# Performance work log

Measured on AMD Instinct MI355X. Metric: run time of the kernel, lower is better.

Reference implementation:

```python
import jax, jax.numpy as jnp
import numpy as np

DIM = 1024
NUM_HEADS = 16
HEAD_DIM = DIM // NUM_HEADS


def setup_inputs() -> dict:
    key = jax.random.key(0)
    k1, k2, k3, k4 = jax.random.split(key, 4)
    x = jax.random.normal(k1, (2, 2048, DIM), dtype=jnp.float32)
    # nn.Linear(dim, 3*dim, bias=False): weight [3*dim, dim], y = x @ W.T
    w_qkv = jax.random.normal(k2, (3 * DIM, DIM), dtype=jnp.float32) * (1.0 / np.sqrt(DIM))
    w_proj = jax.random.normal(k3, (DIM, DIM), dtype=jnp.float32) * (1.0 / np.sqrt(DIM))
    b_proj = jax.random.normal(k4, (DIM,), dtype=jnp.float32) * 0.02
    return {"x": x, "w_qkv": w_qkv, "w_proj": w_proj, "b_proj": b_proj}


def reference(x, w_qkv, w_proj, b_proj):
    B, N, C = x.shape
    H, D = NUM_HEADS, HEAD_DIM
    qkv = jnp.einsum('bnc,oc->bno', x, w_qkv)            # [B,N,3C]
    qkv = qkv.reshape(B, N, 3, H, D)
    q = jnp.transpose(qkv[:, :, 0], (0, 2, 1, 3))        # [B,H,N,D]
    k = jnp.transpose(qkv[:, :, 1], (0, 2, 1, 3))
    v = jnp.transpose(qkv[:, :, 2], (0, 2, 1, 3))
    scale = 1.0 / jnp.sqrt(jnp.asarray(D, dtype=x.dtype))
    scores = jnp.einsum('bhnd,bhmd->bhnm', q, k) * scale  # [B,H,N,N]
    attn = jax.nn.softmax(scores, axis=-1)
    o = jnp.einsum('bhnm,bhmd->bhnd', attn, v)            # [B,H,N,D]
    o = jnp.transpose(o, (0, 2, 1, 3)).reshape(B, N, C)
    return jnp.einsum('bnc,oc->bno', o, w_proj) + b_proj
```

## Files before the change

kernel.cpp:

```cpp
#include <hip/hip_runtime.h>
#include <cmath>

#define DIM 1024
#define NHEADS 16
#define HDIM 64
#define NB 2
#define SEQ 2048

typedef __bf16 bf16x8 __attribute__((ext_vector_type(8)));
typedef __bf16 bf16x4 __attribute__((ext_vector_type(4)));
typedef float f32x4 __attribute__((ext_vector_type(4)));

union Bf8 { bf16x8 v; __bf16 e[8]; unsigned short us[8]; };
union Bf4 { bf16x4 v; __bf16 e[4]; };

__device__ __forceinline__ void split_bf(float f, __bf16 &h, __bf16 &l) {
    h = (__bf16)f;
    l = (__bf16)(f - (float)h);
}
__device__ __forceinline__ unsigned int pack_bf(float f) {
    __bf16 h, l;
    split_bf(f, h, l);
    union { __bf16 b; unsigned short u; } ch, cl;
    ch.b = h; cl.b = l;
    return (unsigned int)ch.u | ((unsigned int)cl.u << 16);
}

__global__ __launch_bounds__(256) void split_f32(const float* __restrict__ in,
                                                 __bf16* __restrict__ hi,
                                                 __bf16* __restrict__ lo, int n4) {
    for (int i = blockIdx.x * blockDim.x + threadIdx.x; i < n4;
         i += gridDim.x * blockDim.x) {
        const float4 v = reinterpret_cast<const float4*>(in)[i];
        const float f[4] = {v.x, v.y, v.z, v.w};
        Bf4 h, l;
#pragma unroll
        for (int e = 0; e < 4; ++e) split_bf(f[e], h.e[e], l.e[e]);
        reinterpret_cast<bf16x4*>(hi)[i] = h.v;
        reinterpret_cast<bf16x4*>(lo)[i] = l.v;
    }
}

template <bool SA, bool SB, bool SOUT, bool QSCALE, bool HAS_BIAS>
__global__ __launch_bounds__(256) void gemm_nt_mfma(
    const float* __restrict__ Af, const __bf16* __restrict__ Agh, const __bf16* __restrict__ Agl,
    const float* __restrict__ Bf, const __bf16* __restrict__ Bgh, const __bf16* __restrict__ Bgl,
    const float* __restrict__ bias,
    float* __restrict__ Cf, __bf16* __restrict__ Cgh, __bf16* __restrict__ Cgl,
    int M, int Nc, int K) {
    __shared__ __align__(16) __bf16 Ah[128][40];
    __shared__ __align__(16) __bf16 Al[128][40];
    __shared__ __align__(16) __bf16 Bh[128][40];
    __shared__ __align__(16) __bf16 Bl[128][40];

    const int nwg  = gridDim.x;
    const int orig = blockIdx.x;
    const int tile = (orig & 7) * (nwg >> 3) + (orig >> 3);
    const int gx   = Nc >> 7;
    const int m0   = (tile / gx) * 128;
    const int n0   = (tile % gx) * 128;

    const int t  = threadIdx.x;
    const int w  = t >> 6;
    const int l  = t & 63;
    const int wr = (w >> 1) * 64;
    const int wc = (w & 1) * 64;
    const int lr = l & 15;
    const int kg = l >> 4;

    const int srow = t >> 1;
    const int skh  = (t & 1) * 16;
    const size_t arow = (size_t)(m0 + srow) * K + skh;
    const size_t brow = (size_t)(n0 + srow) * K + skh;

    f32x4 acc[4][4] = {};

    for (int k0 = 0; k0 < K; k0 += 32) {
        float4 av[4], bv[4];
        bf16x8 sah[2], sal[2], sbh[2], sbl[2];
        if constexpr (SA) {
            sah[0] = *reinterpret_cast<const bf16x8*>(Agh + arow + k0);
            sah[1] = *reinterpret_cast<const bf16x8*>(Agh + arow + k0 + 8);
            sal[0] = *reinterpret_cast<const bf16x8*>(Agl + arow + k0);
            sal[1] = *reinterpret_cast<const bf16x8*>(Agl + arow + k0 + 8);
        } else {
#pragma unroll
            for (int i = 0; i < 4; ++i)
                av[i] = *reinterpret_cast<const float4*>(Af + arow + k0 + i * 4);
        }
        if constexpr (SB) {
            sbh[0] = *reinterpret_cast<const bf16x8*>(Bgh + brow + k0);
            sbh[1] = *reinterpret_cast<const bf16x8*>(Bgh + brow + k0 + 8);
            sbl[0] = *reinterpret_cast<const bf16x8*>(Bgl + brow + k0);
            sbl[1] = *reinterpret_cast<const bf16x8*>(Bgl + brow + k0 + 8);
        } else {
#pragma unroll
            for (int i = 0; i < 4; ++i)
                bv[i] = *reinterpret_cast<const float4*>(Bf + brow + k0 + i * 4);
        }
        __syncthreads();

        if constexpr (SA) {
            *reinterpret_cast<bf16x8*>(&Ah[srow][skh])     = sah[0];
            *reinterpret_cast<bf16x8*>(&Ah[srow][skh + 8]) = sah[1];
            *reinterpret_cast<bf16x8*>(&Al[srow][skh])     = sal[0];
            *reinterpret_cast<bf16x8*>(&Al[srow][skh + 8]) = sal[1];
        } else {
#pragma unroll
            for (int half = 0; half < 2; ++half) {
                Bf8 hh, ll;
#pragma unroll
                for (int q = 0; q < 2; ++q) {
                    const float4 va = av[half * 2 + q];
                    const float fa[4] = {va.x, va.y, va.z, va.w};
#pragma unroll
                    for (int e = 0; e < 4; ++e)
                        split_bf(fa[e], hh.e[q * 4 + e], ll.e[q * 4 + e]);
                }
                *reinterpret_cast<bf16x8*>(&Ah[srow][skh + half * 8]) = hh.v;
                *reinterpret_cast<bf16x8*>(&Al[srow][skh + half * 8]) = ll.v;
            }
        }
        if constexpr (SB) {
            *reinterpret_cast<bf16x8*>(&Bh[srow][skh])     = sbh[0];
            *reinterpret_cast<bf16x8*>(&Bh[srow][skh + 8]) = sbh[1];
            *reinterpret_cast<bf16x8*>(&Bl[srow][skh])     = sbl[0];
            *reinterpret_cast<bf16x8*>(&Bl[srow][skh + 8]) = sbl[1];
        } else {
#pragma unroll
            for (int half = 0; half < 2; ++half) {
                Bf8 hh, ll;
#pragma unroll
                for (int q = 0; q < 2; ++q) {
                    const float4 vb = bv[half * 2 + q];
                    const float fb[4] = {vb.x, vb.y, vb.z, vb.w};
#pragma unroll
                    for (int e = 0; e < 4; ++e)
                        split_bf(fb[e], hh.e[q * 4 + e], ll.e[q * 4 + e]);
                }
                *reinterpret_cast<bf16x8*>(&Bh[srow][skh + half * 8]) = hh.v;
                *reinterpret_cast<bf16x8*>(&Bl[srow][skh + half * 8]) = ll.v;
            }
        }
        __syncthreads();

        bf16x8 fah[4], fal[4], fbh[4], fbl[4];
#pragma unroll
        for (int mi = 0; mi < 4; ++mi) {
            fah[mi] = *reinterpret_cast<const bf16x8*>(&Ah[wr + mi * 16 + lr][kg * 8]);
            fal[mi] = *reinterpret_cast<const bf16x8*>(&Al[wr + mi * 16 + lr][kg * 8]);
        }
#pragma unroll
        for (int nj = 0; nj < 4; ++nj) {
            fbh[nj] = *reinterpret_cast<const bf16x8*>(&Bh[wc + nj * 16 + lr][kg * 8]);
            fbl[nj] = *reinterpret_cast<const bf16x8*>(&Bl[wc + nj * 16 + lr][kg * 8]);
        }
#pragma unroll
        for (int mi = 0; mi < 4; ++mi)
#pragma unroll
            for (int nj = 0; nj < 4; ++nj) {
                acc[mi][nj] = __builtin_amdgcn_mfma_f32_16x16x32_bf16(
                    fah[mi], fbh[nj], acc[mi][nj], 0, 0, 0);
                acc[mi][nj] = __builtin_amdgcn_mfma_f32_16x16x32_bf16(
                    fal[mi], fbh[nj], acc[mi][nj], 0, 0, 0);
                acc[mi][nj] = __builtin_amdgcn_mfma_f32_16x16x32_bf16(
                    fah[mi], fbl[nj], acc[mi][nj], 0, 0, 0);
            }
    }

    const int orw = kg * 4;
#pragma unroll
    for (int mi = 0; mi < 4; ++mi) {
#pragma unroll
        for (int r = 0; r < 4; ++r) {
            const int row = m0 + wr + mi * 16 + orw + r;
#pragma unroll
            for (int nj = 0; nj < 4; ++nj) {
                const int col = n0 + wc + nj * 16 + lr;
                float v = acc[mi][nj][r];
                if constexpr (SOUT) {
                    if constexpr (QSCALE) {
                        if (col < DIM) v *= 0.125f;
                    }
                    __bf16 hh, ll;
                    split_bf(v, hh, ll);
                    const size_t off = (size_t)row * Nc + col;
                    Cgh[off] = hh;
                    Cgl[off] = ll;
                } else {
                    if constexpr (HAS_BIAS) v += bias[col];
                    Cf[(size_t)row * Nc + col] = v;
                }
            }
        }
    }
}

__global__ __launch_bounds__(256, 2) void attn_mfma(const __bf16* __restrict__ qkv_hi,
                                                    const __bf16* __restrict__ qkv_lo,
                                                    __bf16* __restrict__ o_hi,
                                                    __bf16* __restrict__ o_lo) {
    __shared__ __align__(16) __bf16 Khi[64][72];
    __shared__ __align__(16) __bf16 Klo[64][72];
    __shared__ __align__(16) __bf16 Vhi[64][72];
    __shared__ __align__(16) __bf16 Vlo[64][72];
    __shared__ __align__(16) unsigned int P32[128][68];

    const int nwg  = gridDim.x;
    const int orig = blockIdx.x;
    const int tile = (orig & 7) * (nwg >> 3) + (orig >> 3);
    const int qt = tile & 15;
    const int h  = (tile >> 4) & 15;
    const int b  = tile >> 8;

    const int t  = threadIdx.x;
    const int w  = t >> 6;
    const int l  = t & 63;
    const int lr = l & 15;
    const int kg = l >> 4;
    const int wq = w * 32;

    const size_t bbase = (size_t)b * SEQ * 3 * DIM;
    const int    hoff  = h * HDIM;

    bf16x8 qfh[2][2], qfl[2][2];
#pragma unroll
    for (int mi = 0; mi < 2; ++mi) {
#pragma unroll
        for (int ks = 0; ks < 2; ++ks) {
            const size_t qoff = bbase +
                (size_t)(qt * 128 + wq + mi * 16 + lr) * (3 * DIM) + hoff + ks * 32 + kg * 8;
            qfh[mi][ks] = *reinterpret_cast<const bf16x8*>(qkv_hi + qoff);
            qfl[mi][ks] = *reinterpret_cast<const bf16x8*>(qkv_lo + qoff);
        }
    }

    const int skey = t >> 2;
    const int sd0  = (t & 3) * 16;
    const int vkp  = (t & 31) * 2;
    const int vd0  = (t >> 5) * 8;

    const size_t koff  = bbase + DIM + hoff + (size_t)skey * (3 * DIM) + sd0;
    const size_t voff0 = bbase + 2 * DIM + hoff + (size_t)(vkp + 0) * (3 * DIM) + vd0;
    const size_t voff1 = bbase + 2 * DIM + hoff + (size_t)(vkp + 1) * (3 * DIM) + vd0;
    const size_t kvstep = (size_t)64 * 3 * DIM;

    bf16x8 kr[4], vr[4];
    kr[0] = *reinterpret_cast<const bf16x8*>(qkv_hi + koff);
    kr[1] = *reinterpret_cast<const bf16x8*>(qkv_hi + koff + 8);
    kr[2] = *reinterpret_cast<const bf16x8*>(qkv_lo + koff);
    kr[3] = *reinterpret_cast<const bf16x8*>(qkv_lo + koff + 8);
    vr[0] = *reinterpret_cast<const bf16x8*>(qkv_hi + voff0);
    vr[1] = *reinterpret_cast<const bf16x8*>(qkv_hi + voff1);
    vr[2] = *reinterpret_cast<const bf16x8*>(qkv_lo + voff0);
    vr[3] = *reinterpret_cast<const bf16x8*>(qkv_lo + voff1);

    f32x4 oacc[2][4] = {};
    float mrow[2][4], lrow[2][4];
#pragma unroll
    for (int mi = 0; mi < 2; ++mi)
#pragma unroll
        for (int r = 0; r < 4; ++r) { mrow[mi][r] = -INFINITY; lrow[mi][r] = 0.f; }

    for (int kt = 0; kt < SEQ / 64; ++kt) {
        __syncthreads();

        *reinterpret_cast<bf16x8*>(&Khi[skey][sd0])     = kr[0];
        *reinterpret_cast<bf16x8*>(&Khi[skey][sd0 + 8]) = kr[1];
        *reinterpret_cast<bf16x8*>(&Klo[skey][sd0])     = kr[2];
        *reinterpret_cast<bf16x8*>(&Klo[skey][sd0 + 8]) = kr[3];
        {
            Bf8 k0h, k1h, k0l, k1l;
            k0h.v = vr[0]; k1h.v = vr[1]; k0l.v = vr[2]; k1l.v = vr[3];
#pragma unroll
            for (int e = 0; e < 8; ++e) {
                *reinterpret_cast<unsigned int*>(&Vhi[vd0 + e][vkp]) =
                    (unsigned int)k0h.us[e] | ((unsigned int)k1h.us[e] << 16);
                *reinterpret_cast<unsigned int*>(&Vlo[vd0 + e][vkp]) =
                    (unsigned int)k0l.us[e] | ((unsigned int)k1l.us[e] << 16);
            }
        }
        __syncthreads();

        if (kt < SEQ / 64 - 1) {
            const size_t kk = koff + (size_t)(kt + 1) * kvstep;
            const size_t v0 = voff0 + (size_t)(kt + 1) * kvstep;
            const size_t v1 = voff1 + (size_t)(kt + 1) * kvstep;
            kr[0] = *reinterpret_cast<const bf16x8*>(qkv_hi + kk);
            kr[1] = *reinterpret_cast<const bf16x8*>(qkv_hi + kk + 8);
            kr[2] = *reinterpret_cast<const bf16x8*>(qkv_lo + kk);
            kr[3] = *reinterpret_cast<const bf16x8*>(qkv_lo + kk + 8);
            vr[0] = *reinterpret_cast<const bf16x8*>(qkv_hi + v0);
            vr[1] = *reinterpret_cast<const bf16x8*>(qkv_hi + v1);
            vr[2] = *reinterpret_cast<const bf16x8*>(qkv_lo + v0);
            vr[3] = *reinterpret_cast<const bf16x8*>(qkv_lo + v1);
        }

        f32x4 sacc[2][4] = {};
#pragma unroll
        for (int ks = 0; ks < 2; ++ks) {
#pragma unroll
            for (int nj = 0; nj < 4; ++nj) {
                const bf16x8 kh = *reinterpret_cast<const bf16x8*>(&Khi[nj * 16 + lr][ks * 32 + kg * 8]);
                const bf16x8 kl = *reinterpret_cast<const bf16x8*>(&Klo[nj * 16 + lr][ks * 32 + kg * 8]);
#pragma unroll
                for (int mi = 0; mi < 2; ++mi) {
                    sacc[mi][nj] = __builtin_amdgcn_mfma_f32_16x16x32_bf16(qfh[mi][ks], kh, sacc[mi][nj], 0, 0, 0);
                    sacc[mi][nj] = __builtin_amdgcn_mfma_f32_16x16x32_bf16(qfl[mi][ks], kh, sacc[mi][nj], 0, 0, 0);
                    sacc[mi][nj] = __builtin_amdgcn_mfma_f32_16x16x32_bf16(qfh[mi][ks], kl, sacc[mi][nj], 0, 0, 0);
                }
            }
        }

#pragma unroll
        for (int mi = 0; mi < 2; ++mi) {
#pragma unroll
            for (int r = 0; r < 4; ++r) {
                const float s0 = sacc[mi][0][r], s1 = sacc[mi][1][r];
                const float s2 = sacc[mi][2][r], s3 = sacc[mi][3][r];
                float pm = fmaxf(fmaxf(s0, s1), fmaxf(s2, s3));
                pm = fmaxf(pm, __shfl_xor(pm, 1));
                pm = fmaxf(pm, __shfl_xor(pm, 2));
                pm = fmaxf(pm, __shfl_xor(pm, 4));
                pm = fmaxf(pm, __shfl_xor(pm, 8));
                const float nm = fmaxf(mrow[mi][r], pm);
                const float p0 = __expf(s0 - nm), p1 = __expf(s1 - nm);
                const float p2 = __expf(s2 - nm), p3 = __expf(s3 - nm);
                float ls = (p0 + p1) + (p2 + p3);
                ls += __shfl_xor(ls, 1);
                ls += __shfl_xor(ls, 2);
                ls += __shfl_xor(ls, 4);
                ls += __shfl_xor(ls, 8);
                const float fac = __expf(mrow[mi][r] - nm);
                mrow[mi][r] = nm;
                lrow[mi][r] = lrow[mi][r] * fac + ls;
#pragma unroll
                for (int njd = 0; njd < 4; ++njd) oacc[mi][njd][r] *= fac;
                const int prow = wq + mi * 16 + kg * 4 + r;
                P32[prow][0 * 16 + lr] = pack_bf(p0);
                P32[prow][1 * 16 + lr] = pack_bf(p1);
                P32[prow][2 * 16 + lr] = pack_bf(p2);
                P32[prow][3 * 16 + lr] = pack_bf(p3);
            }
        }

#pragma unroll
        for (int ks = 0; ks < 2; ++ks) {
            bf16x8 ph[2], pl[2];
#pragma unroll
            for (int mi = 0; mi < 2; ++mi) {
                const unsigned int* pp = &P32[wq + mi * 16 + lr][ks * 32 + kg * 8];
                const uint4 u0 = *reinterpret_cast<const uint4*>(pp);
                const uint4 u1 = *reinterpret_cast<const uint4*>(pp + 4);
                const unsigned int uu[8] = {u0.x, u0.y, u0.z, u0.w, u1.x, u1.y, u1.z, u1.w};
                Bf8 hh, ll;
#pragma unroll
                for (int j = 0; j < 8; ++j) {
                    hh.us[j] = (unsigned short)(uu[j] & 0xffffu);
                    ll.us[j] = (unsigned short)(uu[j] >> 16);
                }
                ph[mi] = hh.v;
                pl[mi] = ll.v;
            }
#pragma unroll
            for (int njd = 0; njd < 4; ++njd) {
                const bf16x8 vh = *reinterpret_cast<const bf16x8*>(&Vhi[njd * 16 + lr][ks * 32 + kg * 8]);
                const bf16x8 vl = *reinterpret_cast<const bf16x8*>(&Vlo[njd * 16 + lr][ks * 32 + kg * 8]);
#pragma unroll
                for (int mi = 0; mi < 2; ++mi) {
                    oacc[mi][njd] = __builtin_amdgcn_mfma_f32_16x16x32_bf16(ph[mi], vh, oacc[mi][njd], 0, 0, 0);
                    oacc[mi][njd] = __builtin_amdgcn_mfma_f32_16x16x32_bf16(pl[mi], vh, oacc[mi][njd], 0, 0, 0);
                    oacc[mi][njd] = __builtin_amdgcn_mfma_f32_16x16x32_bf16(ph[mi], vl, oacc[mi][njd], 0, 0, 0);
                }
            }
        }
    }

#pragma unroll
    for (int mi = 0; mi < 2; ++mi) {
#pragma unroll
        for (int r = 0; r < 4; ++r) {
            const float inv = 1.f / lrow[mi][r];
            const int grow = b * SEQ + qt * 128 + wq + mi * 16 + kg * 4 + r;
#pragma unroll
            for (int njd = 0; njd < 4; ++njd) {
                const float v = oacc[mi][njd][r] * inv;
                __bf16 hh, ll;
                split_bf(v, hh, ll);
                const size_t off = (size_t)grow * DIM + hoff + njd * 16 + lr;
                o_hi[off] = hh;
                o_lo[off] = ll;
            }
        }
    }
}

extern "C" void kernel_launch(void* const* d_in, const int* in_sizes, int n_in,
                              void* d_out, int out_size, void* d_ws, size_t ws_size,
                              hipStream_t stream) {
    const float* x      = (const float*)d_in[0];
    const float* w_qkv  = (const float*)d_in[1];
    const float* w_proj = (const float*)d_in[2];
    const float* b_proj = (const float*)d_in[3];
    float* out = (float*)d_out;

    const int M = NB * SEQ;
    const size_t qkvN  = (size_t)M * 3 * DIM;
    const size_t obufN = (size_t)M * DIM;
    const size_t xN    = (size_t)M * DIM;
    const size_t wqN   = (size_t)(3 * DIM) * DIM;
    const size_t wpN   = (size_t)DIM * DIM;

    __bf16* p = (__bf16*)d_ws;
    __bf16* qkv_hi = p;  p += qkvN;
    __bf16* qkv_lo = p;  p += qkvN;
    __bf16* ob_hi  = p;  p += obufN;
    __bf16* ob_lo  = p;  p += obufN;
    __bf16* x_hi   = p;  p += xN;
    __bf16* x_lo   = p;  p += xN;
    __bf16* wq_hi  = p;  p += wqN;
    __bf16* wq_lo  = p;  p += wqN;
    __bf16* wp_hi  = p;  p += wpN;
    __bf16* wp_lo  = p;  p += wpN;
    const size_t NEED_FULL = 2 * (qkvN + obufN + xN + wqN + wpN) * sizeof(__bf16);
    const bool full = ws_size >= NEED_FULL;

    if (full) {
        split_f32<<<512, 256, 0, stream>>>(x,      x_hi,  x_lo,  (int)(xN / 4));
        split_f32<<<512, 256, 0, stream>>>(w_qkv,  wq_hi, wq_lo, (int)(wqN / 4));
        split_f32<<<256, 256, 0, stream>>>(w_proj, wp_hi, wp_lo, (int)(wpN / 4));
        gemm_nt_mfma<true, true, true, true, false>
            <<<dim3((M / 128) * (3 * DIM / 128)), 256, 0, stream>>>(
            nullptr, x_hi, x_lo, nullptr, wq_hi, wq_lo,
            nullptr, nullptr, qkv_hi, qkv_lo, M, 3 * DIM, DIM);
    } else {
        gemm_nt_mfma<false, false, true, true, false>
            <<<dim3((M / 128) * (3 * DIM / 128)), 256, 0, stream>>>(
            x, nullptr, nullptr, w_qkv, nullptr, nullptr,
            nullptr, nullptr, qkv_hi, qkv_lo, M, 3 * DIM, DIM);
    }

    attn_mfma<<<dim3((SEQ / 128) * NHEADS * NB), 256, 0, stream>>>(
        qkv_hi, qkv_lo, ob_hi, ob_lo);

    if (full) {
        gemm_nt_mfma<true, true, false, false, true>
            <<<dim3((M / 128) * (DIM / 128)), 256, 0, stream>>>(
            nullptr, ob_hi, ob_lo, nullptr, wp_hi, wp_lo,
            b_proj, out, nullptr, nullptr, M, DIM, DIM);
    } else {
        gemm_nt_mfma<true, false, false, false, true>
            <<<dim3((M / 128) * (DIM / 128)), 256, 0, stream>>>(
            nullptr, ob_hi, ob_lo, w_proj, nullptr, nullptr,
            b_proj, out, nullptr, nullptr, M, DIM, DIM);
    }
}
```

Baseline: 365.6 us.

## Transpose attention MFMAs to keep P in registers and drop LDS staging

Swaps the MFMA operand order so score and output accumulators are transposed, with each lane holding one query row. Row max and sum reductions then need only two cross-lane shuffles per row, and P is rebuilt as an MFMA operand with register shuffles instead of a round trip through LDS. Removing the P32 shared buffer frees LDS, so launch bounds are raised to allow three workgroups per CU. The cost is many __shfl gather operations and possible register pressure under the tighter occupancy bound.

```diff
diff --git a/kernel.cpp b/kernel.cpp
--- a/kernel.cpp
+++ b/kernel.cpp
@@ -13,18 +13,14 @@
 
 union Bf8 { bf16x8 v; __bf16 e[8]; unsigned short us[8]; };
 union Bf4 { bf16x4 v; __bf16 e[4]; };
+union Bf1 { __bf16 b; unsigned short u; };
+union U4B { unsigned int u[4]; bf16x8 v; };
 
 __device__ __forceinline__ void split_bf(float f, __bf16 &h, __bf16 &l) {
     h = (__bf16)f;
     l = (__bf16)(f - (float)h);
 }
-__device__ __forceinline__ unsigned int pack_bf(float f) {
-    __bf16 h, l;
-    split_bf(f, h, l);
-    union { __bf16 b; unsigned short u; } ch, cl;
-    ch.b = h; cl.b = l;
-    return (unsigned int)ch.u | ((unsigned int)cl.u << 16);
-}
+__device__ __forceinline__ unsigned short bfu(__bf16 b) { Bf1 c; c.b = b; return c.u; }
 
 __global__ __launch_bounds__(256) void split_f32(const float* __restrict__ in,
                                                  __bf16* __restrict__ hi,
@@ -196,7 +192,7 @@
     }
 }
 
-__global__ __launch_bounds__(256, 2) void attn_mfma(const __bf16* __restrict__ qkv_hi,
+__global__ __launch_bounds__(256, 3) void attn_mfma(const __bf16* __restrict__ qkv_hi,
                                                     const __bf16* __restrict__ qkv_lo,
                                                     __bf16* __restrict__ o_hi,
                                                     __bf16* __restrict__ o_lo) {
@@ -204,7 +200,6 @@
     __shared__ __align__(16) __bf16 Klo[64][72];
     __shared__ __align__(16) __bf16 Vhi[64][72];
     __shared__ __align__(16) __bf16 Vlo[64][72];
-    __shared__ __align__(16) unsigned int P32[128][68];
 
     const int nwg  = gridDim.x;
     const int orig = blockIdx.x;
@@ -256,11 +251,12 @@
     vr[3] = *reinterpret_cast<const bf16x8*>(qkv_lo + voff1);
 
     f32x4 oacc[2][4] = {};
-    float mrow[2][4], lrow[2][4];
-#pragma unroll
-    for (int mi = 0; mi < 2; ++mi)
-#pragma unroll
-        for (int r = 0; r < 4; ++r) { mrow[mi][r] = -INFINITY; lrow[mi][r] = 0.f; }
+    float mrow[2] = {-INFINITY, -INFINITY};
+    float lrow[2] = {0.f, 0.f};
+
+    const int srcA  = (l & 15) | ((l & 16) << 1);
+    const int srcB  = srcA + 16;
+    const bool selHi = (l & 32) != 0;
 
     for (int kt = 0; kt < SEQ / 64; ++kt) {
         __syncthreads();
@@ -305,62 +301,90 @@
                 const bf16x8 kl = *reinterpret_cast<const bf16x8*>(&Klo[nj * 16 + lr][ks * 32 + kg * 8]);
 #pragma unroll
                 for (int mi = 0; mi < 2; ++mi) {
-                    sacc[mi][nj] = __builtin_amdgcn_mfma_f32_16x16x32_bf16(qfh[mi][ks], kh, sacc[mi][nj], 0, 0, 0);
-                    sacc[mi][nj] = __builtin_amdgcn_mfma_f32_16x16x32_bf16(qfl[mi][ks], kh, sacc[mi][nj], 0, 0, 0);
-                    sacc[mi][nj] = __builtin_amdgcn_mfma_f32_16x16x32_bf16(qfh[mi][ks], kl, sacc[mi][nj], 0, 0, 0);
-                }
-            }
-        }
-
+                    sacc[mi][nj] = __builtin_amdgcn_mfma_f32_16x16x32_bf16(kh, qfh[mi][ks], sacc[mi][nj], 0, 0, 0);
+                    sacc[mi][nj] = __builtin_amdgcn_mfma_f32_16x16x32_bf16(kl, qfh[mi][ks], sacc[mi][nj], 0, 0, 0);
+                    sacc[mi][nj] = __builtin_amdgcn_mfma_f32_16x16x32_bf16(kh, qfl[mi][ks], sacc[mi][nj], 0, 0, 0);
+                }
+            }
+        }
+
+        unsigned int pkh[2][4][2], pkl[2][4][2];
 #pragma unroll
         for (int mi = 0; mi < 2; ++mi) {
-#pragma unroll
-            for (int r = 0; r < 4; ++r) {
-                const float s0 = sacc[mi][0][r], s1 = sacc[mi][1][r];
-                const float s2 = sacc[mi][2][r], s3 = sacc[mi][3][r];
-                float pm = fmaxf(fmaxf(s0, s1), fmaxf(s2, s3));
-                pm = fmaxf(pm, __shfl_xor(pm, 1));
-                pm = fmaxf(pm, __shfl_xor(pm, 2));
-                pm = fmaxf(pm, __shfl_xor(pm, 4));
-                pm = fmaxf(pm, __shfl_xor(pm, 8));
-                const float nm = fmaxf(mrow[mi][r], pm);
-                const float p0 = __expf(s0 - nm), p1 = __expf(s1 - nm);
-                const float p2 = __expf(s2 - nm), p3 = __expf(s3 - nm);
-                float ls = (p0 + p1) + (p2 + p3);
-                ls += __shfl_xor(ls, 1);
-                ls += __shfl_xor(ls, 2);
-                ls += __shfl_xor(ls, 4);
-                ls += __shfl_xor(ls, 8);
-                const float fac = __expf(mrow[mi][r] - nm);
-                mrow[mi][r] = nm;
-                lrow[mi][r] = lrow[mi][r] * fac + ls;
-#pragma unroll
-                for (int njd = 0; njd < 4; ++njd) oacc[mi][njd][r] *= fac;
-                const int prow = wq + mi * 16 + kg * 4 + r;
-                P32[prow][0 * 16 + lr] = pack_bf(p0);
-                P32[prow][1 * 16 + lr] = pack_bf(p1);
-                P32[prow][2 * 16 + lr] = pack_bf(p2);
-                P32[prow][3 * 16 + lr] = pack_bf(p3);
+            float pm = -INFINITY;
+#pragma unroll
+            for (int nj = 0; nj < 4; ++nj)
+#pragma unroll
+                for (int r = 0; r < 4; ++r) pm = fmaxf(pm, sacc[mi][nj][r]);
+            pm = fmaxf(pm, __shfl_xor(pm, 16));
+            pm = fmaxf(pm, __shfl_xor(pm, 32));
+            const float nm = fmaxf(mrow[mi], pm);
+            float ls = 0.f;
+#pragma unroll
+            for (int nj = 0; nj < 4; ++nj)
+#pragma unroll
+                for (int r = 0; r < 4; ++r) {
+                    const float p = __expf(sacc[mi][nj][r] - nm);
+                    sacc[mi][nj][r] = p;
+                    ls += p;
+                }
+            ls += __shfl_xor(ls, 16);
+            ls += __shfl_xor(ls, 32);
+            const float fac = __expf(mrow[mi] - nm);
+            mrow[mi] = nm;
+            lrow[mi] = lrow[mi] * fac + ls;
+#pragma unroll
+            for (int njd = 0; njd < 4; ++njd)
+#pragma unroll
+                for (int r = 0; r < 4; ++r) oacc[mi][njd][r] *= fac;
+#pragma unroll
+            for (int nj = 0; nj < 4; ++nj) {
+                __bf16 hh[4], ll[4];
+#pragma unroll
+                for (int r = 0; r < 4; ++r) split_bf(sacc[mi][nj][r], hh[r], ll[r]);
+                pkh[mi][nj][0] = (unsigned int)bfu(hh[0]) | ((unsigned int)bfu(hh[1]) << 16);
+                pkh[mi][nj][1] = (unsigned int)bfu(hh[2]) | ((unsigned int)bfu(hh[3]) << 16);
+                pkl[mi][nj][0] = (unsigned int)bfu(ll[0]) | ((unsigned int)bfu(ll[1]) << 16);
+                pkl[mi][nj][1] = (unsigned int)bfu(ll[2]) | ((unsigned int)bfu(ll[3]) << 16);
             }
         }
 
 #pragma unroll
         for (int ks = 0; ks < 2; ++ks) {
-            bf16x8 ph[2], pl[2];
+            bf16x8 pbh[2], pbl[2];
 #pragma unroll
             for (int mi = 0; mi < 2; ++mi) {
-                const unsigned int* pp = &P32[wq + mi * 16 + lr][ks * 32 + kg * 8];
-                const uint4 u0 = *reinterpret_cast<const uint4*>(pp);
-                const uint4 u1 = *reinterpret_cast<const uint4*>(pp + 4);
-                const unsigned int uu[8] = {u0.x, u0.y, u0.z, u0.w, u1.x, u1.y, u1.z, u1.w};
-                Bf8 hh, ll;
-#pragma unroll
-                for (int j = 0; j < 8; ++j) {
-                    hh.us[j] = (unsigned short)(uu[j] & 0xffffu);
-                    ll.us[j] = (unsigned short)(uu[j] >> 16);
-                }
-                ph[mi] = hh.v;
-                pl[mi] = ll.v;
+                U4B gh, gl;
+                {
+                    const unsigned int a0 = (unsigned int)__shfl((int)pkh[mi][ks * 2][0], srcA);
+                    const unsigned int a1 = (unsigned int)__shfl((int)pkh[mi][ks * 2 + 1][0], srcA);
+                    const unsigned int b0 = (unsigned int)__shfl((int)pkh[mi][ks * 2][1], srcA);
+                    const unsigned int b1 = (unsigned int)__shfl((int)pkh[mi][ks * 2 + 1][1], srcA);
+                    const unsigned int c0 = (unsigned int)__shfl((int)pkh[mi][ks * 2][0], srcB);
+                    const unsigned int c1 = (unsigned int)__shfl((int)pkh[mi][ks * 2 + 1][0], srcB);
+                    const unsigned int d0 = (unsigned int)__shfl((int)pkh[mi][ks * 2][1], srcB);
+                    const unsigned int d1 = (unsigned int)__shfl((int)pkh[mi][ks * 2 + 1][1], srcB);
+                    gh.u[0] = selHi ? a1 : a0;
+                    gh.u[1] = selHi ? b1 : b0;
+                    gh.u[2] = selHi ? c1 : c0;
+                    gh.u[3] = selHi ? d1 : d0;
+                }
+                {
+                    const unsigned int a0 = (unsigned int)__shfl((int)pkl[mi][ks * 2][0], srcA);
+                    const unsigned int a1 = (unsigned int)__shfl((int)pkl[mi][ks * 2 + 1][0], srcA);
+                    const unsigned int b0 = (unsigned int)__shfl((int)pkl[mi][ks * 2][1], srcA);
+                    const unsigned int b1 = (unsigned int)__shfl((int)pkl[mi][ks * 2 + 1][1], srcA);
+                    const unsigned int c0 = (unsigned int)__shfl((int)pkl[mi][ks * 2][0], srcB);
+                    const unsigned int c1 = (unsigned int)__shfl((int)pkl[mi][ks * 2 + 1][0], srcB);
+                    const unsigned int d0 = (unsigned int)__shfl((int)pkl[mi][ks * 2][1], srcB);
+                    const unsigned int d1 = (unsigned int)__shfl((int)pkl[mi][ks * 2 + 1][1], srcB);
+                    gl.u[0] = selHi ? a1 : a0;
+                    gl.u[1] = selHi ? b1 : b0;
+                    gl.u[2] = selHi ? c1 : c0;
+                    gl.u[3] = selHi ? d1 : d0;
+                }
+                pbh[mi] = gh.v;
+                pbl[mi] = gl.v;
             }
 #pragma unroll
             for (int njd = 0; njd < 4; ++njd) {
@@ -368,9 +392,9 @@
                 const bf16x8 vl = *reinterpret_cast<const bf16x8*>(&Vlo[njd * 16 + lr][ks * 32 + kg * 8]);
 #pragma unroll
                 for (int mi = 0; mi < 2; ++mi) {
-                    oacc[mi][njd] = __builtin_amdgcn_mfma_f32_16x16x32_bf16(ph[mi], vh, oacc[mi][njd], 0, 0, 0);
-                    oacc[mi][njd] = __builtin_amdgcn_mfma_f32_16x16x32_bf16(pl[mi], vh, oacc[mi][njd], 0, 0, 0);
-                    oacc[mi][njd] = __builtin_amdgcn_mfma_f32_16x16x32_bf16(ph[mi], vl, oacc[mi][njd], 0, 0, 0);
+                    oacc[mi][njd] = __builtin_amdgcn_mfma_f32_16x16x32_bf16(vh, pbh[mi], oacc[mi][njd], 0, 0, 0);
+                    oacc[mi][njd] = __builtin_amdgcn_mfma_f32_16x16x32_bf16(vl, pbh[mi], oacc[mi][njd], 0, 0, 0);
+                    oacc[mi][njd] = __builtin_amdgcn_mfma_f32_16x16x32_bf16(vh, pbl[mi], oacc[mi][njd], 0, 0, 0);
                 }
             }
         }
@@ -378,20 +402,19 @@
 
 #pragma unroll
     for (int mi = 0; mi < 2; ++mi) {
-#pragma unroll
-        for (int r = 0; r < 4; ++r) {
-            const float inv = 1.f / lrow[mi][r];
-            const int grow = b * SEQ + qt * 128 + wq + mi * 16 + kg * 4 + r;
-#pragma unroll
-            for (int njd = 0; njd < 4; ++njd) {
+        const float inv = 1.f / lrow[mi];
+        const int grow = b * SEQ + qt * 128 + wq + mi * 16 + lr;
+#pragma unroll
+        for (int njd = 0; njd < 4; ++njd)
+#pragma unroll
+            for (int r = 0; r < 4; ++r) {
                 const float v = oacc[mi][njd][r] * inv;
                 __bf16 hh, ll;
                 split_bf(v, hh, ll);
-                const size_t off = (size_t)grow * DIM + hoff + njd * 16 + lr;
+                const size_t off = (size_t)grow * DIM + hoff + njd * 16 + kg * 4 + r;
                 o_hi[off] = hh;
                 o_lo[off] = ll;
             }
-        }
     }
 }
 
```

Result: slower. 419.6 us (+14.8%).
